# Kernel tuning notes

Measured on AMD Instinct MI355X. Metric: run time of the kernel, lower is better.

Reference implementation:

```python
import jax, jax.numpy as jnp
import numpy as np

DIM = 3
SIGMA_MIN = 0.05
NORM_EPS = 1e-10
DEG2RAD = np.pi / 180.0


def setup_inputs() -> dict:
    key = jax.random.key(0)
    kF, = jax.random.split(key, 1)
    B = 4_000_000
    F = jax.random.normal(kF, (B, 3, 3), dtype=jnp.float32)
    return {
        "F": F,
        "youngs_modulus_log": jnp.asarray(np.log(2_000_000.0), dtype=jnp.float32),
        "poissons_ratio": jnp.asarray(0.4, dtype=jnp.float32),
        "friction_angle": jnp.asarray(25.0, dtype=jnp.float32),
        "cohesion": jnp.asarray(0.0, dtype=jnp.float32),
    }


def reference(F, youngs_modulus_log, poissons_ratio, friction_angle, cohesion):
    E = jnp.exp(youngs_modulus_log)
    sin_phi = jnp.sin(friction_angle * DEG2RAD)
    alpha = jnp.sqrt(2.0 / 3.0) * 2.0 * sin_phi / (3.0 - sin_phi)
    mu = E / (2.0 * (1.0 + poissons_ratio))
    la = E * poissons_ratio / ((1.0 + poissons_ratio) * (1.0 - 2.0 * poissons_ratio))

    # Batched 3x3 SVD: U (B,3,3), sigma (B,3), Vh (B,3,3)
    U, sigma, Vh = jnp.linalg.svd(F, full_matrices=False)

    sigma = jnp.maximum(sigma, SIGMA_MIN)
    eps = jnp.log(sigma)                                   # log strain (B,3)
    trace = eps.sum(axis=1, keepdims=True)                 # (B,1)
    eps_hat = eps - trace / DIM                            # deviatoric part
    eps_hat_norm = jnp.maximum(
        jnp.linalg.norm(eps_hat, axis=1, keepdims=True), NORM_EPS)
    shifted_trace = trace - cohesion * DIM
    cond_yield = shifted_trace < 0.0                       # (B,1)
    delta_gamma = eps_hat_norm + (DIM * la + 2.0 * mu) / (2.0 * mu) * shifted_trace * alpha
    compress_eps = eps - jnp.maximum(delta_gamma, 0.0) / eps_hat_norm * eps_hat
    expand_eps = jnp.ones_like(eps) * cohesion
    eps_corrected = jnp.where(cond_yield, compress_eps, expand_eps)

    # F_corrected = U @ diag(exp(eps_corrected)) @ Vh
    F_corrected = jnp.einsum('bij,bj,bjk->bik', U, jnp.exp(eps_corrected), Vh)
    return F_corrected
```

## Files before the change

### kernel.cpp

```cpp
#include <hip/hip_runtime.h>
#include <math.h>

#define BLOCK 256

__device__ __forceinline__ float frcp(float x) { return __builtin_amdgcn_rcpf(x); }
__device__ __forceinline__ float frsq(float x) { return __builtin_amdgcn_rsqf(x); }

__device__ __forceinline__ void onesided_rot(
    float& x0, float& x1, float& x2,
    float& y0, float& y1, float& y2,
    float& p0, float& p1, float& p2,
    float& q0, float& q1, float& q2)
{
    float app = fmaf(x0, x0, fmaf(x1, x1, x2 * x2));
    float aqq = fmaf(y0, y0, fmaf(y1, y1, y2 * y2));
    float apq = fmaf(x0, y0, fmaf(x1, y1, x2 * y2));
    float del = app - aqq;
    float rho = apq + apq;
    float r   = sqrtf(fmaf(del, del, rho * rho));
    float ch = fabsf(del) + r;
    float sh = (del < 0.0f) ? -rho : rho;
    float n2 = fmaf(ch, ch, sh * sh);
    float inv = frsq(n2);
    bool ok = n2 > 1e-30f;
    float c = ok ? ch * inv : 1.0f;
    float s = ok ? sh * inv : 0.0f;
    bool sw = del < 0.0f;
    float cf = sw ? -s : c;
    float sf = sw ?  c : s;
    float t;
    t = x0; x0 = fmaf(cf, t, sf * y0); y0 = fmaf(cf, y0, -sf * t);
    t = x1; x1 = fmaf(cf, t, sf * y1); y1 = fmaf(cf, y1, -sf * t);
    t = x2; x2 = fmaf(cf, t, sf * y2); y2 = fmaf(cf, y2, -sf * t);
    t = p0; p0 = fmaf(cf, t, sf * q0); q0 = fmaf(cf, q0, -sf * t);
    t = p1; p1 = fmaf(cf, t, sf * q1); q1 = fmaf(cf, q1, -sf * t);
    t = p2; p2 = fmaf(cf, t, sf * q2); q2 = fmaf(cf, q2, -sf * t);
}

__global__ __launch_bounds__(BLOCK) void dp_kernel(
    const float* __restrict__ F,
    const float* __restrict__ p_yml,
    const float* __restrict__ p_nu,
    const float* __restrict__ p_fa,
    const float* __restrict__ p_coh,
    float* __restrict__ out,
    int n_elem)
{
    __shared__ float lds[BLOCK * 9];
    const int t_id = threadIdx.x;
    const long long base_f = (long long)blockIdx.x * (BLOCK * 9);
    const long long nfloats = (long long)n_elem * 9LL;

    #pragma unroll
    for (int j = 0; j < 3; ++j) {
        int idx = t_id + j * BLOCK;
        if (idx < (BLOCK * 9) / 4) {
            long long g4 = base_f / 4 + idx;
            long long gf = g4 * 4;
            if (gf + 3 < nfloats) {
                ((float4*)lds)[idx] = ((const float4*)F)[g4];
            } else {
                #pragma unroll
                for (int k = 0; k < 4; ++k)
                    if (gf + k < nfloats) lds[idx * 4 + k] = F[gf + k];
            }
        }
    }
    __syncthreads();

    const long long e = (long long)blockIdx.x * BLOCK + t_id;
    const bool valid = e < n_elem;

    float a00, a01, a02, a10, a11, a12, a20, a21, a22;
    {
        const float* p = lds + t_id * 9;
        a00 = p[0]; a01 = p[1]; a02 = p[2];
        a10 = p[3]; a11 = p[4]; a12 = p[5];
        a20 = p[6]; a21 = p[7]; a22 = p[8];
    }
    __syncthreads();

    const float yml = p_yml[0];
    const float nu  = p_nu[0];
    const float fa  = p_fa[0];
    const float coh = p_coh[0];
    const float E     = __expf(yml);
    const float sphi  = __sinf(fa * 0.017453292519943295f);
    const float alpha = 1.632993161855452f * sphi * frcp(3.0f - sphi);
    const float mu    = E * 0.5f * frcp(1.0f + nu);
    const float la    = E * nu * frcp((1.0f + nu) * (1.0f - 2.0f * nu));
    const float ratio = (3.0f * la + 2.0f * mu) * frcp(2.0f * mu) * alpha;

    float v00=1.f,v01=0.f,v02=0.f, v10=0.f,v11=1.f,v12=0.f, v20=0.f,v21=0.f,v22=1.f;
    #pragma unroll
    for (int sweep = 0; sweep < 4; ++sweep) {
        onesided_rot(a00,a10,a20, a01,a11,a21, v00,v10,v20, v01,v11,v21);
        onesided_rot(a00,a10,a20, a02,a12,a22, v00,v10,v20, v02,v12,v22);
        onesided_rot(a01,a11,a21, a02,a12,a22, v01,v11,v21, v02,v12,v22);
    }

    float n0sq = fmaf(a00,a00, fmaf(a10,a10, a20*a20));
    float n1sq = fmaf(a01,a01, fmaf(a11,a11, a21*a21));
    float i0 = frsq(fmaxf(n0sq, 1e-30f));
    float i1 = frsq(fmaxf(n1sq, 1e-30f));
    float u00 = a00*i0, u10 = a10*i0, u20 = a20*i0;
    float u01 = a01*i1, u11 = a11*i1, u21 = a21*i1;
    float sig0 = n0sq * i0;
    float sig1 = n1sq * i1;
    float u02 = fmaf(u10, u21, -u20*u11);
    float u12 = fmaf(u20, u01, -u00*u21);
    float u22 = fmaf(u00, u11, -u10*u01);
    float d3  = fmaf(u02, a02, fmaf(u12, a12, u22*a22));
    float sig2 = fabsf(d3);

    float e0 = __logf(fmaxf(sig0, 0.05f));
    float e1 = __logf(fmaxf(sig1, 0.05f));
    float e2 = __logf(fmaxf(sig2, 0.05f));
    float tr  = e0 + e1 + e2;
    float tr3 = tr * (1.0f / 3.0f);
    float h0 = e0 - tr3, h1 = e1 - tr3, h2 = e2 - tr3;
    float hn = sqrtf(fmaf(h0,h0, fmaf(h1,h1, h2*h2)));
    hn = fmaxf(hn, 1e-10f);
    float st = tr - coh * 3.0f;
    float dg = hn + ratio * st;
    float sc = fmaxf(dg, 0.0f) * frcp(hn);
    bool yield = st < 0.0f;
    float ec0 = yield ? fmaf(-sc, h0, e0) : coh;
    float ec1 = yield ? fmaf(-sc, h1, e1) : coh;
    float ec2 = yield ? fmaf(-sc, h2, e2) : coh;
    float f0 = __expf(ec0);
    float f1 = __expf(ec1);
    float f2 = copysignf(__expf(ec2), d3);

    float w00 = u00*f0, w01 = u01*f1, w02 = u02*f2;
    float w10 = u10*f0, w11 = u11*f1, w12 = u12*f2;
    float w20 = u20*f0, w21 = u21*f1, w22 = u22*f2;
    float r00 = fmaf(w00,v00, fmaf(w01,v01, w02*v02));
    float r01 = fmaf(w00,v10, fmaf(w01,v11, w02*v12));
    float r02 = fmaf(w00,v20, fmaf(w01,v21, w02*v22));
    float r10 = fmaf(w10,v00, fmaf(w11,v01, w12*v02));
    float r11 = fmaf(w10,v10, fmaf(w11,v11, w12*v12));
    float r12 = fmaf(w10,v20, fmaf(w11,v21, w12*v22));
    float r20 = fmaf(w20,v00, fmaf(w21,v01, w22*v02));
    float r21 = fmaf(w20,v10, fmaf(w21,v11, w22*v12));
    float r22 = fmaf(w20,v20, fmaf(w21,v21, w22*v22));

    if (valid) {
        float* p = lds + t_id * 9;
        p[0]=r00; p[1]=r01; p[2]=r02;
        p[3]=r10; p[4]=r11; p[5]=r12;
        p[6]=r20; p[7]=r21; p[8]=r22;
    }
    __syncthreads();

    #pragma unroll
    for (int j = 0; j < 3; ++j) {
        int idx = t_id + j * BLOCK;
        if (idx < (BLOCK * 9) / 4) {
            long long g4 = base_f / 4 + idx;
            long long gf = g4 * 4;
            if (gf + 3 < nfloats) {
                ((float4*)out)[g4] = ((float4*)lds)[idx];
            } else {
                #pragma unroll
                for (int k = 0; k < 4; ++k)
                    if (gf + k < nfloats) out[gf + k] = lds[idx * 4 + k];
            }
        }
    }
}

extern "C" void kernel_launch(void* const* d_in, const int* in_sizes, int n_in,
                              void* d_out, int out_size, void* d_ws, size_t ws_size,
                              hipStream_t stream) {
    const float* F = (const float*)d_in[0];
    const int n_elem = in_sizes[0] / 9;
    const int grid = (n_elem + BLOCK - 1) / BLOCK;
    dp_kernel<<<grid, BLOCK, 0, stream>>>(
        F,
        (const float*)d_in[1], (const float*)d_in[2],
        (const float*)d_in[3], (const float*)d_in[4],
        (float*)d_out, n_elem);
}
```

Baseline: 275.0 us.

## Drop V accumulation in Jacobi SVD and track column norms incrementally

The one-sided Jacobi sweeps no longer rotate the V matrix alongside A. Column squared norms are now updated with a closed-form eigenvalue formula instead of being recomputed each rotation. V is rebuilt afterwards from A^T U, with normalization and a cross product, and the third singular value comes from u2^T A v2. This removes many FMAs per rotation across 12 rotations. The cost is extra work after the sweeps and possible accuracy loss from the incremental norms and the reconstructed V, especially for near-degenerate singular values.

```diff
diff --git a/kernel.cpp b/kernel.cpp
--- a/kernel.cpp
+++ b/kernel.cpp
@@ -6,23 +6,19 @@
 __device__ __forceinline__ float frcp(float x) { return __builtin_amdgcn_rcpf(x); }
 __device__ __forceinline__ float frsq(float x) { return __builtin_amdgcn_rsqf(x); }
 
-__device__ __forceinline__ void onesided_rot(
-    float& x0, float& x1, float& x2,
-    float& y0, float& y1, float& y2,
-    float& p0, float& p1, float& p2,
-    float& q0, float& q1, float& q2)
+__device__ __forceinline__ void rot(
+    float& x0, float& x1, float& x2, float& np,
+    float& y0, float& y1, float& y2, float& nq)
 {
-    float app = fmaf(x0, x0, fmaf(x1, x1, x2 * x2));
-    float aqq = fmaf(y0, y0, fmaf(y1, y1, y2 * y2));
     float apq = fmaf(x0, y0, fmaf(x1, y1, x2 * y2));
-    float del = app - aqq;
+    float del = np - nq;
     float rho = apq + apq;
     float r   = sqrtf(fmaf(del, del, rho * rho));
-    float ch = fabsf(del) + r;
-    float sh = (del < 0.0f) ? -rho : rho;
-    float n2 = fmaf(ch, ch, sh * sh);
-    float inv = frsq(n2);
-    bool ok = n2 > 1e-30f;
+    float ch  = fabsf(del) + r;
+    float sh  = (del < 0.0f) ? -rho : rho;
+    float nn  = fmaf(ch, ch, sh * sh);
+    float inv = frsq(nn);
+    bool ok = nn > 1e-30f;
     float c = ok ? ch * inv : 1.0f;
     float s = ok ? sh * inv : 0.0f;
     bool sw = del < 0.0f;
@@ -32,9 +28,9 @@
     t = x0; x0 = fmaf(cf, t, sf * y0); y0 = fmaf(cf, y0, -sf * t);
     t = x1; x1 = fmaf(cf, t, sf * y1); y1 = fmaf(cf, y1, -sf * t);
     t = x2; x2 = fmaf(cf, t, sf * y2); y2 = fmaf(cf, y2, -sf * t);
-    t = p0; p0 = fmaf(cf, t, sf * q0); q0 = fmaf(cf, q0, -sf * t);
-    t = p1; p1 = fmaf(cf, t, sf * q1); q1 = fmaf(cf, q1, -sf * t);
-    t = p2; p2 = fmaf(cf, t, sf * q2); q2 = fmaf(cf, q2, -sf * t);
+    float sum = np + nq;
+    np = 0.5f * (sum + r);
+    nq = fmaxf(0.5f * (sum - r), 0.0f);
 }
 
 __global__ __launch_bounds__(BLOCK) void dp_kernel(
@@ -91,27 +87,53 @@
     const float la    = E * nu * frcp((1.0f + nu) * (1.0f - 2.0f * nu));
     const float ratio = (3.0f * la + 2.0f * mu) * frcp(2.0f * mu) * alpha;
 
-    float v00=1.f,v01=0.f,v02=0.f, v10=0.f,v11=1.f,v12=0.f, v20=0.f,v21=0.f,v22=1.f;
+    float c00=a00, c10=a10, c20=a20;
+    float c01=a01, c11=a11, c21=a21;
+    float c02=a02, c12=a12, c22=a22;
+    float n0 = fmaf(c00,c00, fmaf(c10,c10, c20*c20));
+    float n1 = fmaf(c01,c01, fmaf(c11,c11, c21*c21));
+    float n2 = fmaf(c02,c02, fmaf(c12,c12, c22*c22));
+
     #pragma unroll
     for (int sweep = 0; sweep < 4; ++sweep) {
-        onesided_rot(a00,a10,a20, a01,a11,a21, v00,v10,v20, v01,v11,v21);
-        onesided_rot(a00,a10,a20, a02,a12,a22, v00,v10,v20, v02,v12,v22);
-        onesided_rot(a01,a11,a21, a02,a12,a22, v01,v11,v21, v02,v12,v22);
-    }
-
-    float n0sq = fmaf(a00,a00, fmaf(a10,a10, a20*a20));
-    float n1sq = fmaf(a01,a01, fmaf(a11,a11, a21*a21));
-    float i0 = frsq(fmaxf(n0sq, 1e-30f));
-    float i1 = frsq(fmaxf(n1sq, 1e-30f));
-    float u00 = a00*i0, u10 = a10*i0, u20 = a20*i0;
-    float u01 = a01*i1, u11 = a11*i1, u21 = a21*i1;
-    float sig0 = n0sq * i0;
-    float sig1 = n1sq * i1;
-    float u02 = fmaf(u10, u21, -u20*u11);
-    float u12 = fmaf(u20, u01, -u00*u21);
-    float u22 = fmaf(u00, u11, -u10*u01);
-    float d3  = fmaf(u02, a02, fmaf(u12, a12, u22*a22));
-    float sig2 = fabsf(d3);
+        rot(c00,c10,c20,n0, c01,c11,c21,n1);
+        rot(c00,c10,c20,n0, c02,c12,c22,n2);
+        rot(c01,c11,c21,n1, c02,c12,c22,n2);
+    }
+
+    float i0 = frsq(fmaxf(n0, 1e-30f));
+    float i1 = frsq(fmaxf(n1, 1e-30f));
+    float u00 = c00*i0, u10 = c10*i0, u20 = c20*i0;
+    float u01 = c01*i1, u11 = c11*i1, u21 = c21*i1;
+    float sig0 = n0 * i0;
+    float sig1 = n1 * i1;
+    float u02 = fmaf(u10,u21, -u20*u11);
+    float u12 = fmaf(u20,u01, -u00*u21);
+    float u22 = fmaf(u00,u11, -u10*u01);
+
+    float q0 = fmaf(a00,u00, fmaf(a10,u10, a20*u20));
+    float q1 = fmaf(a01,u00, fmaf(a11,u10, a21*u20));
+    float q2 = fmaf(a02,u00, fmaf(a12,u10, a22*u20));
+    float m0 = fmaf(q0,q0, fmaf(q1,q1, q2*q2));
+    float j0 = frsq(fmaxf(m0, 1e-30f));
+    float v00 = q0*j0, v10 = q1*j0, v20 = q2*j0;
+
+    q0 = fmaf(a00,u01, fmaf(a10,u11, a20*u21));
+    q1 = fmaf(a01,u01, fmaf(a11,u11, a21*u21));
+    q2 = fmaf(a02,u01, fmaf(a12,u11, a22*u21));
+    float m1 = fmaf(q0,q0, fmaf(q1,q1, q2*q2));
+    float j1 = frsq(fmaxf(m1, 1e-30f));
+    float v01 = q0*j1, v11 = q1*j1, v21 = q2*j1;
+
+    float v02 = fmaf(v10,v21, -v20*v11);
+    float v12 = fmaf(v20,v01, -v00*v21);
+    float v22 = fmaf(v00,v11, -v10*v01);
+
+    float w0 = fmaf(a00,v02, fmaf(a01,v12, a02*v22));
+    float w1 = fmaf(a10,v02, fmaf(a11,v12, a12*v22));
+    float w2 = fmaf(a20,v02, fmaf(a21,v12, a22*v22));
+    float s2 = fmaf(u02,w0, fmaf(u12,w1, u22*w2));
+    float sig2 = fabsf(s2);
 
     float e0 = __logf(fmaxf(sig0, 0.05f));
     float e1 = __logf(fmaxf(sig1, 0.05f));
@@ -130,7 +152,7 @@
     float ec2 = yield ? fmaf(-sc, h2, e2) : coh;
     float f0 = __expf(ec0);
     float f1 = __expf(ec1);
-    float f2 = copysignf(__expf(ec2), d3);
+    float f2 = copysignf(__expf(ec2), s2);
 
     float w00 = u00*f0, w01 = u01*f1, w02 = u02*f2;
     float w10 = u10*f0, w11 = u11*f1, w12 = u12*f2;
```

New measurement: 270.0 us. Within noise of the previous version (-1.8%).
